# Optimization experiments

Hardware: AMD Instinct MI355X
Metric: run time of the kernel (lower is better)

## Reference

```python
import jax, jax.numpy as jnp
import numpy as np

B, M, K = 32, 64, 36
DS, DX, DQ, H = 512, 128, 512, 256


def setup_inputs() -> dict:
    key = jax.random.key(0)
    ks = jax.random.split(key, 11)
    sc = lambda fan_in: 1.0 / np.sqrt(fan_in)
    return {
        "s2": jax.random.normal(ks[0], (B, M, DS), jnp.float32),
        "x0": jax.random.normal(ks[1], (B, K, DX), jnp.float32),
        "q": jax.random.normal(ks[2], (B, DQ), jnp.float32),
        # score MLP: Linear(DS+DX+DQ -> H), ReLU, Linear(H -> 1)
        "score_w1": jax.random.normal(ks[3], (DS + DX + DQ, H), jnp.float32) * sc(DS + DX + DQ),
        "score_b1": jax.random.normal(ks[4], (H,), jnp.float32) * 0.01,
        "score_w2": jax.random.normal(ks[5], (H, 1), jnp.float32) * sc(H),
        "score_b2": jax.random.normal(ks[6], (1,), jnp.float32) * 0.01,
        # h MLP: Linear(DS -> H), ReLU, Linear(H -> DX)
        "h_w1": jax.random.normal(ks[7], (DS, H), jnp.float32) * sc(DS),
        "h_b1": jax.random.normal(ks[8], (H,), jnp.float32) * 0.01,
        "h_w2": jax.random.normal(ks[9], (H, DX), jnp.float32) * sc(H),
        "h_b2": jax.random.normal(ks[10], (DX,), jnp.float32) * 0.01,
    }


def reference(s2, x0, q, score_w1, score_b1, score_w2, score_b2, h_w1, h_b1, h_w2, h_b2):
    ds = s2.shape[-1]
    dx = x0.shape[-1]
    # First score Linear over concat [s_exp, x_exp, q_exp] decomposes into
    # block matmuls (same math as Linear on the concat, no 4D concat tensor).
    w_s = score_w1[:ds]            # (DS, H)
    w_x = score_w1[ds:ds + dx]     # (DX, H)
    w_q = score_w1[ds + dx:]       # (DQ, H)
    pre_s = jnp.einsum('bmd,dh->bmh', s2, w_s)   # (b, m, H)
    pre_x = jnp.einsum('bkd,dh->bkh', x0, w_x)   # (b, k, H)
    pre_q = q @ w_q                              # (b, H)
    hidden = jax.nn.relu(pre_s[:, :, None, :] + pre_x[:, None, :, :]
                         + pre_q[:, None, None, :] + score_b1)  # (b, m, k, H)
    logits = jnp.einsum('bmkh,h->bmk', hidden, score_w2[:, 0]) + score_b2[0]
    att = jax.nn.softmax(logits, axis=1)         # softmax over m
    h_s = jax.nn.relu(s2 @ h_w1 + h_b1) @ h_w2 + h_b2  # (b, m, DX)
    agg = jnp.einsum('bmk,bmf->bkf', att, h_s)   # (b, k, DX)
    return jnp.concatenate([x0, agg], axis=-1)   # (b, k, 2*DX)
```

## Files before the change

### kernel.cpp

```cpp
#include <hip/hip_runtime.h>

#define B_  32
#define M_  64
#define K_  36
#define DS_ 512
#define DX_ 128
#define DQ_ 512
#define H_  256

#define TMA  16
#define DCH  128

__global__ __launch_bounds__(256) void kernA(
    const float* __restrict__ s2,
    const float* __restrict__ score_w1,
    const float* __restrict__ h_w1,
    const float* __restrict__ q,
    const float* __restrict__ score_b1,
    float* __restrict__ pre_s,
    float* __restrict__ ph1,
    float* __restrict__ qpre)
{
    const int t   = threadIdx.x;
    const int bid = blockIdx.x;

    if (bid >= 1024) {
        const int b = bid - 1024;
        const float* qp = q + (size_t)b * DQ_;
        const float* wq = score_w1 + (size_t)(DS_ + DX_) * H_ + t;
        float a0 = score_b1[t], a1 = 0.f, a2 = 0.f, a3 = 0.f;
        for (int d = 0; d < DQ_; d += 4) {
            const float4 q4 = *(const float4*)(qp + d);
            a0 = fmaf(q4.x, wq[(size_t)(d + 0) * H_], a0);
            a1 = fmaf(q4.y, wq[(size_t)(d + 1) * H_], a1);
            a2 = fmaf(q4.z, wq[(size_t)(d + 2) * H_], a2);
            a3 = fmaf(q4.w, wq[(size_t)(d + 3) * H_], a3);
        }
        qpre[(size_t)b * H_ + t] = (a0 + a1) + (a2 + a3);
        return;
    }

    const int tile = bid >> 3;
    const int mat  = bid & 1;
    const int dq   = (bid >> 1) & 3;

    const float* w  = (mat ? h_w1 : score_w1) + (size_t)(dq * DCH) * H_ + t;
    const float* sp = s2 + (size_t)tile * TMA * DS_ + dq * DCH;

    float acc[TMA];
    #pragma unroll
    for (int i = 0; i < TMA; ++i) acc[i] = 0.f;

    for (int d = 0; d < DCH; d += 4) {
        const float w0 = w[(size_t)(d + 0) * H_];
        const float w1 = w[(size_t)(d + 1) * H_];
        const float w2v = w[(size_t)(d + 2) * H_];
        const float w3 = w[(size_t)(d + 3) * H_];
        #pragma unroll
        for (int i = 0; i < TMA; ++i) {
            const float4 s4 = *(const float4*)(sp + (size_t)i * DS_ + d);
            acc[i] = fmaf(s4.x, w0, acc[i]);
            acc[i] = fmaf(s4.y, w1, acc[i]);
            acc[i] = fmaf(s4.z, w2v, acc[i]);
            acc[i] = fmaf(s4.w, w3, acc[i]);
        }
    }

    float* dst = (mat ? ph1 : pre_s) + (size_t)tile * TMA * H_ + t;
    #pragma unroll
    for (int i = 0; i < TMA; ++i)
        atomicAdd(dst + (size_t)i * H_, acc[i]);
}

__global__ __launch_bounds__(256) void kernC(
    const float* __restrict__ pre_s,
    const float* __restrict__ ph1,
    const float* __restrict__ qpre,
    const float* __restrict__ score_w1,
    const float* __restrict__ score_w2,
    const float* __restrict__ h_b1,
    const float* __restrict__ h_w2,
    const float* __restrict__ h_b2,
    const float* __restrict__ x0,
    float* __restrict__ out)
{
    __shared__ float cw[H_];
    __shared__ float w2s[H_];
    __shared__ float logit[M_];
    __shared__ float att[M_];
    __shared__ float part[DX_];

    const int t  = threadIdx.x;
    const int bk = blockIdx.x;
    const int b  = bk / K_;
    const float* x0p = x0 + (size_t)bk * DX_;

    w2s[t] = score_w2[t];
    {
        const float* wx = score_w1 + (size_t)DS_ * H_ + t;
        float a0 = qpre[(size_t)b * H_ + t], a1 = 0.f, a2 = 0.f, a3 = 0.f;
        for (int d = 0; d < DX_; d += 4) {
            const float4 x4 = *(const float4*)(x0p + d);
            a0 = fmaf(x4.x, wx[(size_t)(d + 0) * H_], a0);
            a1 = fmaf(x4.y, wx[(size_t)(d + 1) * H_], a1);
            a2 = fmaf(x4.z, wx[(size_t)(d + 2) * H_], a2);
            a3 = fmaf(x4.w, wx[(size_t)(d + 3) * H_], a3);
        }
        cw[t] = (a0 + a1) + (a2 + a3);
    }
    __syncthreads();

    const int wave = t >> 6, lane = t & 63;
    const float c0 = cw[lane],        c1 = cw[lane + 64],
                c2 = cw[lane + 128],  c3 = cw[lane + 192];
    const float v0 = w2s[lane],       v1 = w2s[lane + 64],
                v2 = w2s[lane + 128], v3 = w2s[lane + 192];

    const float* ps = pre_s + (size_t)b * M_ * H_;
    #pragma unroll 2
    for (int mi = 0; mi < M_ / 4 / 2; ++mi) {
        const int m0 = wave * (M_ / 4) + mi * 2;
        const float* p0 = ps + (size_t)m0 * H_;
        const float* p1 = p0 + H_;
        float pa = fmaxf(p0[lane]       + c0, 0.f) * v0
                 + fmaxf(p0[lane + 64]  + c1, 0.f) * v1
                 + fmaxf(p0[lane + 128] + c2, 0.f) * v2
                 + fmaxf(p0[lane + 192] + c3, 0.f) * v3;
        float pb = fmaxf(p1[lane]       + c0, 0.f) * v0
                 + fmaxf(p1[lane + 64]  + c1, 0.f) * v1
                 + fmaxf(p1[lane + 128] + c2, 0.f) * v2
                 + fmaxf(p1[lane + 192] + c3, 0.f) * v3;
        #pragma unroll
        for (int off = 32; off > 0; off >>= 1) {
            pa += __shfl_down(pa, off, 64);
            pb += __shfl_down(pb, off, 64);
        }
        if (lane == 0) { logit[m0] = pa; logit[m0 + 1] = pb; }
    }
    __syncthreads();

    if (wave == 0) {
        const float L = logit[lane];
        float mx = L;
        #pragma unroll
        for (int off = 32; off > 0; off >>= 1)
            mx = fmaxf(mx, __shfl_xor(mx, off, 64));
        const float e = expf(L - mx);
        float s = e;
        #pragma unroll
        for (int off = 32; off > 0; off >>= 1)
            s += __shfl_xor(s, off, 64);
        att[lane] = e / s;
    }
    __syncthreads();

    {
        const float* hp = ph1 + (size_t)b * M_ * H_ + t;
        const float b1v = h_b1[t];
        float r0 = 0.f, r1 = 0.f;
        #pragma unroll 4
        for (int m = 0; m < M_; m += 2) {
            r0 = fmaf(att[m],     fmaxf(hp[(size_t)m * H_] + b1v, 0.f), r0);
            r1 = fmaf(att[m + 1], fmaxf(hp[(size_t)(m + 1) * H_] + b1v, 0.f), r1);
        }
        cw[t] = r0 + r1;
    }
    __syncthreads();

    const int f  = t & 127;
    const int hh = t >> 7;
    const float* wp = h_w2 + (size_t)(hh * 128) * DX_ + f;
    float a0 = 0.f, a1 = 0.f, a2 = 0.f, a3 = 0.f;
    for (int h = 0; h < 128; h += 4) {
        a0 = fmaf(cw[hh * 128 + h + 0], wp[(size_t)(h + 0) * DX_], a0);
        a1 = fmaf(cw[hh * 128 + h + 1], wp[(size_t)(h + 1) * DX_], a1);
        a2 = fmaf(cw[hh * 128 + h + 2], wp[(size_t)(h + 2) * DX_], a2);
        a3 = fmaf(cw[hh * 128 + h + 3], wp[(size_t)(h + 3) * DX_], a3);
    }
    const float sum = (a0 + a1) + (a2 + a3);
    if (hh) part[f] = sum;
    __syncthreads();

    float* o = out + (size_t)bk * (2 * DX_);
    if (!hh) {
        o[DX_ + f] = sum + part[f] + h_b2[f];
    } else {
        o[f] = x0p[f];
    }
}

extern "C" void kernel_launch(void* const* d_in, const int* in_sizes, int n_in,
                              void* d_out, int out_size, void* d_ws, size_t ws_size,
                              hipStream_t stream) {
    (void)in_sizes; (void)n_in; (void)out_size; (void)ws_size;
    const float* s2       = (const float*)d_in[0];
    const float* x0       = (const float*)d_in[1];
    const float* q        = (const float*)d_in[2];
    const float* score_w1 = (const float*)d_in[3];
    const float* score_b1 = (const float*)d_in[4];
    const float* score_w2 = (const float*)d_in[5];
    const float* h_w1     = (const float*)d_in[7];
    const float* h_b1     = (const float*)d_in[8];
    const float* h_w2     = (const float*)d_in[9];
    const float* h_b2     = (const float*)d_in[10];
    float* out = (float*)d_out;

    float* ws    = (float*)d_ws;
    float* pre_s = ws;
    float* ph1   = ws + (size_t)B_ * M_ * H_;
    float* qpre  = ph1 + (size_t)B_ * M_ * H_;

    hipMemsetAsync(d_ws, 0, (size_t)2 * B_ * M_ * H_ * sizeof(float), stream);

    kernA<<<1056, 256, 0, stream>>>(s2, score_w1, h_w1, q, score_b1,
                                    pre_s, ph1, qpre);
    kernC<<<B_ * K_, 256, 0, stream>>>(pre_s, ph1, qpre, score_w1, score_w2,
                                       h_b1, h_w2, h_b2, x0, out);
}
```

Baseline: 131.1 us.

## Replace atomic split-K with in-block LDS reduction and drop workspace memset

kernA now splits the 512-wide reduction across two halves of a 512-thread block and combines them through shared memory. This lets it store results directly instead of using global atomicAdd, which also removes the hipMemsetAsync launch. The row tile shrinks from 16 to 8 and the grid is halved. kernC replaces the per-row wave shuffle reductions for the score logits with a padded shared-memory transpose that wave 0 then sums. Costs are fewer concurrent blocks and more register pressure from 512-thread blocks.

Measured after the change: 178.6 us. 1.36x slower.

```diff
diff --git a/kernel.cpp b/kernel.cpp
--- a/kernel.cpp
+++ b/kernel.cpp
@@ -8,10 +8,9 @@
 #define DQ_ 512
 #define H_  256
 
-#define TMA  16
-#define DCH  128
-
-__global__ __launch_bounds__(256) void kernA(
+#define TMA 8
+
+__global__ __launch_bounds__(512) void kernA(
     const float* __restrict__ s2,
     const float* __restrict__ score_w1,
     const float* __restrict__ h_w1,
@@ -21,37 +20,42 @@
     float* __restrict__ ph1,
     float* __restrict__ qpre)
 {
+    __shared__ float lsum[TMA][H_];
     const int t   = threadIdx.x;
     const int bid = blockIdx.x;
 
-    if (bid >= 1024) {
-        const int b = bid - 1024;
-        const float* qp = q + (size_t)b * DQ_;
-        const float* wq = score_w1 + (size_t)(DS_ + DX_) * H_ + t;
-        float a0 = score_b1[t], a1 = 0.f, a2 = 0.f, a3 = 0.f;
-        for (int d = 0; d < DQ_; d += 4) {
-            const float4 q4 = *(const float4*)(qp + d);
-            a0 = fmaf(q4.x, wq[(size_t)(d + 0) * H_], a0);
-            a1 = fmaf(q4.y, wq[(size_t)(d + 1) * H_], a1);
-            a2 = fmaf(q4.z, wq[(size_t)(d + 2) * H_], a2);
-            a3 = fmaf(q4.w, wq[(size_t)(d + 3) * H_], a3);
-        }
-        qpre[(size_t)b * H_ + t] = (a0 + a1) + (a2 + a3);
+    if (bid >= 512) {
+        if (t < H_) {
+            const int b = bid - 512;
+            const float* qp = q + (size_t)b * DQ_;
+            const float* wq = score_w1 + (size_t)(DS_ + DX_) * H_ + t;
+            float a0 = score_b1[t], a1 = 0.f, a2 = 0.f, a3 = 0.f;
+            for (int d = 0; d < DQ_; d += 4) {
+                const float4 q4 = *(const float4*)(qp + d);
+                a0 = fmaf(q4.x, wq[(size_t)(d + 0) * H_], a0);
+                a1 = fmaf(q4.y, wq[(size_t)(d + 1) * H_], a1);
+                a2 = fmaf(q4.z, wq[(size_t)(d + 2) * H_], a2);
+                a3 = fmaf(q4.w, wq[(size_t)(d + 3) * H_], a3);
+            }
+            qpre[(size_t)b * H_ + t] = (a0 + a1) + (a2 + a3);
+        }
         return;
     }
 
-    const int tile = bid >> 3;
+    const int tile = bid >> 1;
     const int mat  = bid & 1;
-    const int dq   = (bid >> 1) & 3;
-
-    const float* w  = (mat ? h_w1 : score_w1) + (size_t)(dq * DCH) * H_ + t;
-    const float* sp = s2 + (size_t)tile * TMA * DS_ + dq * DCH;
+    const int ks   = t >> 8;
+    const int h    = t & (H_ - 1);
+
+    const float* w  = (mat ? h_w1 : score_w1) + (size_t)(ks * 256) * H_ + h;
+    const float* sp = s2 + (size_t)tile * TMA * DS_ + ks * 256;
 
     float acc[TMA];
     #pragma unroll
     for (int i = 0; i < TMA; ++i) acc[i] = 0.f;
 
-    for (int d = 0; d < DCH; d += 4) {
+    #pragma unroll 4
+    for (int d = 0; d < 256; d += 4) {
         const float w0 = w[(size_t)(d + 0) * H_];
         const float w1 = w[(size_t)(d + 1) * H_];
         const float w2v = w[(size_t)(d + 2) * H_];
@@ -66,10 +70,17 @@
         }
     }
 
-    float* dst = (mat ? ph1 : pre_s) + (size_t)tile * TMA * H_ + t;
-    #pragma unroll
-    for (int i = 0; i < TMA; ++i)
-        atomicAdd(dst + (size_t)i * H_, acc[i]);
+    if (ks) {
+        #pragma unroll
+        for (int i = 0; i < TMA; ++i) lsum[i][h] = acc[i];
+    }
+    __syncthreads();
+    if (!ks) {
+        float* dst = (mat ? ph1 : pre_s) + (size_t)tile * TMA * H_ + h;
+        #pragma unroll
+        for (int i = 0; i < TMA; ++i)
+            dst[(size_t)i * H_] = acc[i] + lsum[i][h];
+    }
 }
 
 __global__ __launch_bounds__(256) void kernC(
@@ -84,9 +95,9 @@
     const float* __restrict__ x0,
     float* __restrict__ out)
 {
+    __shared__ float red[M_][65];
     __shared__ float cw[H_];
     __shared__ float w2s[H_];
-    __shared__ float logit[M_];
     __shared__ float att[M_];
     __shared__ float part[DX_];
 
@@ -117,30 +128,27 @@
                 v2 = w2s[lane + 128], v3 = w2s[lane + 192];
 
     const float* ps = pre_s + (size_t)b * M_ * H_;
-    #pragma unroll 2
-    for (int mi = 0; mi < M_ / 4 / 2; ++mi) {
-        const int m0 = wave * (M_ / 4) + mi * 2;
-        const float* p0 = ps + (size_t)m0 * H_;
-        const float* p1 = p0 + H_;
-        float pa = fmaxf(p0[lane]       + c0, 0.f) * v0
-                 + fmaxf(p0[lane + 64]  + c1, 0.f) * v1
-                 + fmaxf(p0[lane + 128] + c2, 0.f) * v2
-                 + fmaxf(p0[lane + 192] + c3, 0.f) * v3;
-        float pb = fmaxf(p1[lane]       + c0, 0.f) * v0
-                 + fmaxf(p1[lane + 64]  + c1, 0.f) * v1
-                 + fmaxf(p1[lane + 128] + c2, 0.f) * v2
-                 + fmaxf(p1[lane + 192] + c3, 0.f) * v3;
-        #pragma unroll
-        for (int off = 32; off > 0; off >>= 1) {
-            pa += __shfl_down(pa, off, 64);
-            pb += __shfl_down(pb, off, 64);
-        }
-        if (lane == 0) { logit[m0] = pa; logit[m0 + 1] = pb; }
+    #pragma unroll 4
+    for (int mi = 0; mi < M_ / 4; ++mi) {
+        const int m = wave * (M_ / 4) + mi;
+        const float* p = ps + (size_t)m * H_;
+        red[m][lane] = fmaxf(p[lane]       + c0, 0.f) * v0
+                     + fmaxf(p[lane + 64]  + c1, 0.f) * v1
+                     + fmaxf(p[lane + 128] + c2, 0.f) * v2
+                     + fmaxf(p[lane + 192] + c3, 0.f) * v3;
     }
     __syncthreads();
 
     if (wave == 0) {
-        const float L = logit[lane];
+        float a0 = 0.f, a1 = 0.f, a2 = 0.f, a3 = 0.f;
+        #pragma unroll 4
+        for (int l = 0; l < 64; l += 4) {
+            a0 += red[lane][l + 0];
+            a1 += red[lane][l + 1];
+            a2 += red[lane][l + 2];
+            a3 += red[lane][l + 3];
+        }
+        const float L = (a0 + a1) + (a2 + a3);
         float mx = L;
         #pragma unroll
         for (int off = 32; off > 0; off >>= 1)
@@ -171,11 +179,11 @@
     const int hh = t >> 7;
     const float* wp = h_w2 + (size_t)(hh * 128) * DX_ + f;
     float a0 = 0.f, a1 = 0.f, a2 = 0.f, a3 = 0.f;
-    for (int h = 0; h < 128; h += 4) {
-        a0 = fmaf(cw[hh * 128 + h + 0], wp[(size_t)(h + 0) * DX_], a0);
-        a1 = fmaf(cw[hh * 128 + h + 1], wp[(size_t)(h + 1) * DX_], a1);
-        a2 = fmaf(cw[hh * 128 + h + 2], wp[(size_t)(h + 2) * DX_], a2);
-        a3 = fmaf(cw[hh * 128 + h + 3], wp[(size_t)(h + 3) * DX_], a3);
+    for (int hcv = 0; hcv < 128; hcv += 4) {
+        a0 = fmaf(cw[hh * 128 + hcv + 0], wp[(size_t)(hcv + 0) * DX_], a0);
+        a1 = fmaf(cw[hh * 128 + hcv + 1], wp[(size_t)(hcv + 1) * DX_], a1);
+        a2 = fmaf(cw[hh * 128 + hcv + 2], wp[(size_t)(hcv + 2) * DX_], a2);
+        a3 = fmaf(cw[hh * 128 + hcv + 3], wp[(size_t)(hcv + 3) * DX_], a3);
     }
     const float sum = (a0 + a1) + (a2 + a3);
     if (hh) part[f] = sum;
@@ -210,10 +218,8 @@
     float* ph1   = ws + (size_t)B_ * M_ * H_;
     float* qpre  = ph1 + (size_t)B_ * M_ * H_;
 
-    hipMemsetAsync(d_ws, 0, (size_t)2 * B_ * M_ * H_ * sizeof(float), stream);
-
-    kernA<<<1056, 256, 0, stream>>>(s2, score_w1, h_w1, q, score_b1,
-                                    pre_s, ph1, qpre);
+    kernA<<<544, 512, 0, stream>>>(s2, score_w1, h_w1, q, score_b1,
+                                   pre_s, ph1, qpre);
     kernC<<<B_ * K_, 256, 0, stream>>>(pre_s, ph1, qpre, score_w1, score_w2,
                                        h_b1, h_w2, h_b2, x0, out);
 }
```

## Precompute h MLP per row and x/q projections, slim attention kernel

Applied to the files above, without the earlier changes.

Moves the x0 projection (plus q pre-activation) into the first kernel's extra blocks, computing a per-(b,k) bias vector, and adds a new kernel that applies the h MLP second layer to all B*M rows once instead of per (b,k) block. The final kernel then only computes logits with vectorized loads and an LDS transpose-reduce, a softmax, and an attention-weighted sum over the precomputed h_s rows. This removes redundant per-k recomputation of the h_w2 matvec and the x0 projection, at the cost of an extra kernel launch, a larger memset, and more atomics.

After: 139.5 us. 1.06x slower.

```diff
diff --git a/kernel.cpp b/kernel.cpp
--- a/kernel.cpp
+++ b/kernel.cpp
@@ -10,6 +10,7 @@
 
 #define TMA  16
 #define DCH  128
+#define KB   9
 
 __global__ __launch_bounds__(256) void kernA(
     const float* __restrict__ s2,
@@ -17,15 +18,18 @@
     const float* __restrict__ h_w1,
     const float* __restrict__ q,
     const float* __restrict__ score_b1,
+    const float* __restrict__ x0,
     float* __restrict__ pre_s,
     float* __restrict__ ph1,
-    float* __restrict__ qpre)
+    float* __restrict__ cvec)
 {
     const int t   = threadIdx.x;
     const int bid = blockIdx.x;
 
     if (bid >= 1024) {
-        const int b = bid - 1024;
+        const int cb = bid - 1024;
+        const int b  = cb >> 2;
+        const int kq = cb & 3;
         const float* qp = q + (size_t)b * DQ_;
         const float* wq = score_w1 + (size_t)(DS_ + DX_) * H_ + t;
         float a0 = score_b1[t], a1 = 0.f, a2 = 0.f, a3 = 0.f;
@@ -36,7 +40,31 @@
             a2 = fmaf(q4.z, wq[(size_t)(d + 2) * H_], a2);
             a3 = fmaf(q4.w, wq[(size_t)(d + 3) * H_], a3);
         }
-        qpre[(size_t)b * H_ + t] = (a0 + a1) + (a2 + a3);
+        const float qacc = (a0 + a1) + (a2 + a3);
+
+        float acc[KB];
+        #pragma unroll
+        for (int kk = 0; kk < KB; ++kk) acc[kk] = qacc;
+
+        const float* xsrc = x0 + ((size_t)b * K_ + kq * KB) * DX_;
+        const float* wx   = score_w1 + (size_t)DS_ * H_ + t;
+        for (int d = 0; d < DX_; d += 4) {
+            const float w0 = wx[(size_t)(d + 0) * H_];
+            const float w1 = wx[(size_t)(d + 1) * H_];
+            const float w2v = wx[(size_t)(d + 2) * H_];
+            const float w3 = wx[(size_t)(d + 3) * H_];
+            #pragma unroll
+            for (int kk = 0; kk < KB; ++kk) {
+                const float4 x4 = *(const float4*)(xsrc + (size_t)kk * DX_ + d);
+                acc[kk] = fmaf(x4.x, w0, acc[kk]);
+                acc[kk] = fmaf(x4.y, w1, acc[kk]);
+                acc[kk] = fmaf(x4.z, w2v, acc[kk]);
+                acc[kk] = fmaf(x4.w, w3, acc[kk]);
+            }
+        }
+        #pragma unroll
+        for (int kk = 0; kk < KB; ++kk)
+            cvec[((size_t)b * K_ + kq * KB + kk) * H_ + t] = acc[kk];
         return;
     }
 
@@ -72,75 +100,88 @@
         atomicAdd(dst + (size_t)i * H_, acc[i]);
 }
 
+__global__ __launch_bounds__(256) void kernH(
+    const float* __restrict__ ph1,
+    const float* __restrict__ h_b1,
+    const float* __restrict__ h_w2,
+    float* __restrict__ h_s)
+{
+    __shared__ float sh[4][DCH];
+    const int t    = threadIdx.x;
+    const int tile = blockIdx.x >> 1;
+    const int hh   = blockIdx.x & 1;
+    const int r0   = tile * 4;
+
+    if (t < 128) {
+        const int row = t >> 5, j4 = (t & 31) * 4;
+        const float4 p = *(const float4*)(ph1 + (size_t)(r0 + row) * H_ + hh * DCH + j4);
+        const float4 b = *(const float4*)(h_b1 + hh * DCH + j4);
+        float4 r;
+        r.x = fmaxf(p.x + b.x, 0.f);
+        r.y = fmaxf(p.y + b.y, 0.f);
+        r.z = fmaxf(p.z + b.z, 0.f);
+        r.w = fmaxf(p.w + b.w, 0.f);
+        *(float4*)&sh[row][j4] = r;
+    }
+    __syncthreads();
+
+    const int f  = t & 127;
+    const int rp = t >> 7;
+    const float* wp = h_w2 + (size_t)(hh * DCH) * DX_ + f;
+    float acc0 = 0.f, acc1 = 0.f;
+    #pragma unroll 4
+    for (int h = 0; h < DCH; ++h) {
+        const float wv = wp[(size_t)h * DX_];
+        acc0 = fmaf(sh[rp * 2 + 0][h], wv, acc0);
+        acc1 = fmaf(sh[rp * 2 + 1][h], wv, acc1);
+    }
+    atomicAdd(h_s + (size_t)(r0 + rp * 2 + 0) * DX_ + f, acc0);
+    atomicAdd(h_s + (size_t)(r0 + rp * 2 + 1) * DX_ + f, acc1);
+}
+
 __global__ __launch_bounds__(256) void kernC(
     const float* __restrict__ pre_s,
-    const float* __restrict__ ph1,
-    const float* __restrict__ qpre,
-    const float* __restrict__ score_w1,
+    const float* __restrict__ h_s,
+    const float* __restrict__ cvec,
     const float* __restrict__ score_w2,
-    const float* __restrict__ h_b1,
-    const float* __restrict__ h_w2,
     const float* __restrict__ h_b2,
     const float* __restrict__ x0,
     float* __restrict__ out)
 {
-    __shared__ float cw[H_];
-    __shared__ float w2s[H_];
-    __shared__ float logit[M_];
-    __shared__ float att[M_];
-    __shared__ float part[DX_];
-
-    const int t  = threadIdx.x;
-    const int bk = blockIdx.x;
-    const int b  = bk / K_;
-    const float* x0p = x0 + (size_t)bk * DX_;
-
-    w2s[t] = score_w2[t];
-    {
-        const float* wx = score_w1 + (size_t)DS_ * H_ + t;
-        float a0 = qpre[(size_t)b * H_ + t], a1 = 0.f, a2 = 0.f, a3 = 0.f;
-        for (int d = 0; d < DX_; d += 4) {
-            const float4 x4 = *(const float4*)(x0p + d);
-            a0 = fmaf(x4.x, wx[(size_t)(d + 0) * H_], a0);
-            a1 = fmaf(x4.y, wx[(size_t)(d + 1) * H_], a1);
-            a2 = fmaf(x4.z, wx[(size_t)(d + 2) * H_], a2);
-            a3 = fmaf(x4.w, wx[(size_t)(d + 3) * H_], a3);
-        }
-        cw[t] = (a0 + a1) + (a2 + a3);
-    }
-    __syncthreads();
-
+    __shared__ float  red[M_][65];
+    __shared__ float  att[M_];
+    __shared__ float4 part[8][32];
+
+    const int t    = threadIdx.x;
+    const int bk   = blockIdx.x;
+    const int b    = bk / K_;
     const int wave = t >> 6, lane = t & 63;
-    const float c0 = cw[lane],        c1 = cw[lane + 64],
-                c2 = cw[lane + 128],  c3 = cw[lane + 192];
-    const float v0 = w2s[lane],       v1 = w2s[lane + 64],
-                v2 = w2s[lane + 128], v3 = w2s[lane + 192];
+
+    const float4 cf = *(const float4*)(cvec + (size_t)bk * H_ + 4 * lane);
+    const float4 wf = *(const float4*)(score_w2 + 4 * lane);
 
     const float* ps = pre_s + (size_t)b * M_ * H_;
-    #pragma unroll 2
-    for (int mi = 0; mi < M_ / 4 / 2; ++mi) {
-        const int m0 = wave * (M_ / 4) + mi * 2;
-        const float* p0 = ps + (size_t)m0 * H_;
-        const float* p1 = p0 + H_;
-        float pa = fmaxf(p0[lane]       + c0, 0.f) * v0
-                 + fmaxf(p0[lane + 64]  + c1, 0.f) * v1
-                 + fmaxf(p0[lane + 128] + c2, 0.f) * v2
-                 + fmaxf(p0[lane + 192] + c3, 0.f) * v3;
-        float pb = fmaxf(p1[lane]       + c0, 0.f) * v0
-                 + fmaxf(p1[lane + 64]  + c1, 0.f) * v1
-                 + fmaxf(p1[lane + 128] + c2, 0.f) * v2
-                 + fmaxf(p1[lane + 192] + c3, 0.f) * v3;
-        #pragma unroll
-        for (int off = 32; off > 0; off >>= 1) {
-            pa += __shfl_down(pa, off, 64);
-            pb += __shfl_down(pb, off, 64);
-        }
-        if (lane == 0) { logit[m0] = pa; logit[m0 + 1] = pb; }
+    #pragma unroll 4
+    for (int mi = 0; mi < M_ / 4; ++mi) {
+        const int m = wave * (M_ / 4) + mi;
+        const float4 p = *(const float4*)(ps + (size_t)m * H_ + 4 * lane);
+        red[m][lane] = fmaxf(p.x + cf.x, 0.f) * wf.x
+                     + fmaxf(p.y + cf.y, 0.f) * wf.y
+                     + fmaxf(p.z + cf.z, 0.f) * wf.z
+                     + fmaxf(p.w + cf.w, 0.f) * wf.w;
     }
     __syncthreads();
 
     if (wave == 0) {
-        const float L = logit[lane];
+        float a0 = 0.f, a1 = 0.f, a2 = 0.f, a3 = 0.f;
+        #pragma unroll 4
+        for (int l = 0; l < 64; l += 4) {
+            a0 += red[lane][l + 0];
+            a1 += red[lane][l + 1];
+            a2 += red[lane][l + 2];
+            a3 += red[lane][l + 3];
+        }
+        const float L = (a0 + a1) + (a2 + a3);
         float mx = L;
         #pragma unroll
         for (int off = 32; off > 0; off >>= 1)
@@ -155,37 +196,36 @@
     __syncthreads();
 
     {
-        const float* hp = ph1 + (size_t)b * M_ * H_ + t;
-        const float b1v = h_b1[t];
-        float r0 = 0.f, r1 = 0.f;
-        #pragma unroll 4
-        for (int m = 0; m < M_; m += 2) {
-            r0 = fmaf(att[m],     fmaxf(hp[(size_t)m * H_] + b1v, 0.f), r0);
-            r1 = fmaf(att[m + 1], fmaxf(hp[(size_t)(m + 1) * H_] + b1v, 0.f), r1);
-        }
-        cw[t] = r0 + r1;
-    }
-    __syncthreads();
-
-    const int f  = t & 127;
-    const int hh = t >> 7;
-    const float* wp = h_w2 + (size_t)(hh * 128) * DX_ + f;
-    float a0 = 0.f, a1 = 0.f, a2 = 0.f, a3 = 0.f;
-    for (int h = 0; h < 128; h += 4) {
-        a0 = fmaf(cw[hh * 128 + h + 0], wp[(size_t)(h + 0) * DX_], a0);
-        a1 = fmaf(cw[hh * 128 + h + 1], wp[(size_t)(h + 1) * DX_], a1);
-        a2 = fmaf(cw[hh * 128 + h + 2], wp[(size_t)(h + 2) * DX_], a2);
-        a3 = fmaf(cw[hh * 128 + h + 3], wp[(size_t)(h + 3) * DX_], a3);
-    }
-    const float sum = (a0 + a1) + (a2 + a3);
-    if (hh) part[f] = sum;
-    __syncthreads();
-
-    float* o = out + (size_t)bk * (2 * DX_);
-    if (!hh) {
-        o[DX_ + f] = sum + part[f] + h_b2[f];
-    } else {
-        o[f] = x0p[f];
+        const int g = t >> 5, l32 = t & 31;
+        const float* hp = h_s + ((size_t)b * M_ + g * 8) * DX_ + 4 * l32;
+        float4 acc = make_float4(0.f, 0.f, 0.f, 0.f);
+        #pragma unroll
+        for (int j = 0; j < 8; ++j) {
+            const float a = att[g * 8 + j];
+            const float4 hv = *(const float4*)(hp + (size_t)j * DX_);
+            acc.x = fmaf(a, hv.x, acc.x);
+            acc.y = fmaf(a, hv.y, acc.y);
+            acc.z = fmaf(a, hv.z, acc.z);
+            acc.w = fmaf(a, hv.w, acc.w);
+        }
+        part[g][l32] = acc;
+    }
+    __syncthreads();
+
+    const float4* x04 = (const float4*)(x0 + (size_t)bk * DX_);
+    float4* o4 = (float4*)(out + (size_t)bk * 2 * DX_);
+    if (t < 32) {
+        float4 s = part[0][t];
+        #pragma unroll
+        for (int j = 1; j < 8; ++j) {
+            const float4 p = part[j][t];
+            s.x += p.x; s.y += p.y; s.z += p.z; s.w += p.w;
+        }
+        const float4 b2 = *(const float4*)(h_b2 + 4 * t);
+        s.x += b2.x; s.y += b2.y; s.z += b2.z; s.w += b2.w;
+        o4[32 + t] = s;
+    } else if (t < 64) {
+        o4[t - 32] = x04[t - 32];
     }
 }
 
@@ -207,13 +247,16 @@
 
     float* ws    = (float*)d_ws;
     float* pre_s = ws;
-    float* ph1   = ws + (size_t)B_ * M_ * H_;
-    float* qpre  = ph1 + (size_t)B_ * M_ * H_;
-
-    hipMemsetAsync(d_ws, 0, (size_t)2 * B_ * M_ * H_ * sizeof(float), stream);
-
-    kernA<<<1056, 256, 0, stream>>>(s2, score_w1, h_w1, q, score_b1,
-                                    pre_s, ph1, qpre);
-    kernC<<<B_ * K_, 256, 0, stream>>>(pre_s, ph1, qpre, score_w1, score_w2,
-                                       h_b1, h_w2, h_b2, x0, out);
-}
+    float* ph1   = pre_s + (size_t)B_ * M_ * H_;
+    float* h_s   = ph1   + (size_t)B_ * M_ * H_;
+    float* cvec  = h_s   + (size_t)B_ * M_ * DX_;
+
+    hipMemsetAsync(d_ws, 0,
+                   (size_t)B_ * M_ * (H_ + H_ + DX_) * sizeof(float), stream);
+
+    kernA<<<1152, 256, 0, stream>>>(s2, score_w1, h_w1, q, score_b1, x0,
+                                    pre_s, ph1, cvec);
+    kernH<<<1024, 256, 0, stream>>>(ph1, h_b1, h_w2, h_s);
+    kernC<<<B_ * K_, 256, 0, stream>>>(pre_s, h_s, cvec, score_w2, h_b2,
+                                       x0, out);
+}
```
